# Performance work log

Hardware: AMD Instinct MI355X
Metric: run time of the kernel (lower is better)

Reference implementation:

```python
import jax, jax.numpy as jnp
import numpy as np

HIDDEN = 1024
HEADS = 16
HEAD_DIM = HIDDEN // HEADS


def setup_inputs() -> dict:
    key = jax.random.key(0)
    ks = jax.random.split(key, 9)
    B, S = 4, 2048
    s = 1.0 / np.sqrt(HIDDEN)
    return {
        "inputs": jax.random.normal(ks[0], (B, S, HIDDEN), dtype=jnp.float32),
        "Wq": jax.random.normal(ks[1], (HIDDEN, HIDDEN), dtype=jnp.float32) * s,
        "bq": jnp.zeros((HIDDEN,), dtype=jnp.float32),
        "Wk": jax.random.normal(ks[2], (HIDDEN, HIDDEN), dtype=jnp.float32) * s,
        "bk": jnp.zeros((HIDDEN,), dtype=jnp.float32),
        "Wv": jax.random.normal(ks[3], (HIDDEN, HIDDEN), dtype=jnp.float32) * s,
        "bv": jnp.zeros((HIDDEN,), dtype=jnp.float32),
        "Wp": jax.random.normal(ks[4], (HIDDEN, HIDDEN), dtype=jnp.float32) * s,
        "bp": jnp.zeros((HIDDEN,), dtype=jnp.float32),
        "heads_z": jnp.ones((1, HEADS, 1, 1), dtype=jnp.float32),
        "hidden_z": jnp.ones((HIDDEN,), dtype=jnp.float32),
    }


def _split_heads(x):
    # [B,S,HIDDEN] -> [B,H,S,Dh]
    B, S, _ = x.shape
    return x.reshape(B, S, HEADS, HEAD_DIM).transpose(0, 2, 1, 3)


def reference(inputs, Wq, bq, Wk, bk, Wv, bv, Wp, bp, heads_z, hidden_z):
    q = _split_heads(inputs @ Wq.T + bq)
    k = _split_heads(inputs @ Wk.T + bk)
    v = _split_heads(inputs @ Wv.T + bv)
    scores = jnp.einsum("bhqd,bhkd->bhqk", q, k) / jnp.sqrt(
        jnp.asarray(HEAD_DIM, dtype=q.dtype))
    probs = jax.nn.softmax(scores, axis=-1)
    ctx = jnp.einsum("bhqk,bhkd->bhqd", probs, v)  # [B,H,S,Dh]
    ctx = ctx * heads_z
    B, H, S, D = ctx.shape
    ctx = ctx.transpose(0, 2, 1, 3).reshape(B, S, H * D)
    out = ctx @ Wp.T + bp
    out = out * hidden_z
    return out
```

## Files before the change

kernel.cpp:

```cpp
#include <hip/hip_runtime.h>
#include <hip/hip_bf16.h>

#define HID 1024
#define NH 16
#define DH 64
#define SEQ 2048
#define NB 4
#define MTOT (NB*SEQ)

typedef __attribute__((ext_vector_type(4))) float f32x4;
typedef __attribute__((ext_vector_type(8))) __bf16 bf16x8;
typedef __attribute__((ext_vector_type(4))) __bf16 bf16x4;

__device__ __forceinline__ f32x4 mfma16(bf16x8 a, bf16x8 b, f32x4 c) {
    return __builtin_amdgcn_mfma_f32_16x16x32_bf16(a, b, c, 0, 0, 0);
}

__device__ __forceinline__ void gload16(const void* g, void* l) {
    __builtin_amdgcn_global_load_lds(
        (const __attribute__((address_space(1))) unsigned int*)g,
        (__attribute__((address_space(3))) unsigned int*)l, 16, 0, 0);
}

__device__ __forceinline__ float fexp2(float x) {
#if __has_builtin(__builtin_amdgcn_exp2f)
    return __builtin_amdgcn_exp2f(x);
#else
    return exp2f(x);
#endif
}

__global__ __launch_bounds__(256)
void cvt(const float* __restrict__ in, __bf16* __restrict__ out, int n) {
    int i = (blockIdx.x * 256 + threadIdx.x) * 4;
    if (i >= n) return;
    float4 v = *(const float4*)(in + i);
    bf16x4 o = { (__bf16)v.x, (__bf16)v.y, (__bf16)v.z, (__bf16)v.w };
    *(bf16x4*)(out + i) = o;
}

template<int MODE>
__global__ __launch_bounds__(256)
void gemm_bt(const __bf16* __restrict__ A, const __bf16* __restrict__ W,
             const float* __restrict__ bias, const float* __restrict__ hz,
             void* __restrict__ outp)
{
    __shared__ __bf16 As[128 * 32];
    __shared__ __bf16 Bs[128 * 32];
    const int tid  = threadIdx.x;
    const int lane = tid & 63, wid = tid >> 6;
    const int m0 = blockIdx.x * 128;
    const int n0 = blockIdx.y * 128;
    const int wm = (wid >> 1) * 64, wn = (wid & 1) * 64;

    f32x4 acc[4][4];
    #pragma unroll
    for (int i = 0; i < 4; i++)
        #pragma unroll
        for (int j = 0; j < 4; j++) acc[i][j] = (f32x4){0.f, 0.f, 0.f, 0.f};

    for (int kt = 0; kt < HID; kt += 32) {
        #pragma unroll
        for (int i = 0; i < 2; i++) {
            int c = wid * 128 + i * 64 + lane;
            int row = c >> 2, slot = c & 3;
            int ss = slot ^ (row & 3);
            gload16(A + (size_t)(m0 + row) * HID + kt + ss * 8, (char*)As + c * 16);
            gload16(W + (size_t)(n0 + row) * HID + kt + ss * 8, (char*)Bs + c * 16);
        }
        __syncthreads();

        bf16x8 af[4], bfr[4];
        #pragma unroll
        for (int mi = 0; mi < 4; mi++) {
            int row = wm + mi * 16 + (lane & 15);
            int off = row * 64 + (((lane >> 4) * 16) ^ ((row & 3) << 4));
            af[mi] = *(const bf16x8*)((const char*)As + off);
        }
        #pragma unroll
        for (int ni = 0; ni < 4; ni++) {
            int row = wn + ni * 16 + (lane & 15);
            int off = row * 64 + (((lane >> 4) * 16) ^ ((row & 3) << 4));
            bfr[ni] = *(const bf16x8*)((const char*)Bs + off);
        }
        #pragma unroll
        for (int mi = 0; mi < 4; mi++)
            #pragma unroll
            for (int ni = 0; ni < 4; ni++)
                acc[mi][ni] = mfma16(af[mi], bfr[ni], acc[mi][ni]);
        __syncthreads();
    }

    #pragma unroll
    for (int mi = 0; mi < 4; mi++)
        #pragma unroll
        for (int ni = 0; ni < 4; ni++)
            #pragma unroll
            for (int r = 0; r < 4; r++) {
                int m = m0 + wm + mi * 16 + ((lane >> 4) * 4) + r;
                int n = n0 + wn + ni * 16 + (lane & 15);
                float v = acc[mi][ni][r] + bias[n];
                if (MODE == 3) {
                    ((float*)outp)[(size_t)m * HID + n] = v * hz[n];
                } else {
                    int b = m >> 11, s = m & (SEQ - 1);
                    int h = n >> 6,  d = n & 63;
                    size_t idx;
                    if (MODE == 2) idx = ((size_t)(b * NH + h) * DH + d) * SEQ + s;
                    else           idx = ((size_t)(b * NH + h) * SEQ + s) * DH + d;
                    ((__bf16*)outp)[idx] = (__bf16)v;
                }
            }
}

#define KVB 64
#define SM_SCALE 0.18033688f

__global__ __launch_bounds__(512, 4)
void attn(const __bf16* __restrict__ Q, const __bf16* __restrict__ K,
          const __bf16* __restrict__ VT, const float* __restrict__ heads_z,
          __bf16* __restrict__ C)
{
    __shared__ __bf16 Ks[2][KVB * 64];
    __shared__ __bf16 Vs[2][KVB * 64];
    __shared__ __bf16 Ps[8][32 * 64];
    const int tid = threadIdx.x, lane = tid & 63, wid = tid >> 6;
    const int qb = blockIdx.x, h = blockIdx.y, b = blockIdx.z;
    const size_t bh = (size_t)(b * NH + h);
    const __bf16* Qg = Q + bh * SEQ * DH;
    const __bf16* Kg = K + bh * SEQ * DH;
    const __bf16* Vg = VT + bh * (size_t)DH * SEQ;
    const int q0 = qb * 256;

    bf16x8 qa[2][2];
    #pragma unroll
    for (int mi = 0; mi < 2; mi++)
        #pragma unroll
        for (int kf = 0; kf < 2; kf++) {
            int row = q0 + wid * 32 + mi * 16 + (lane & 15);
            qa[mi][kf] = *(const bf16x8*)(Qg + (size_t)row * DH + kf * 32 + (lane >> 4) * 8);
        }

    f32x4 ctx[2][4];
    float mrun[2] = {-1e30f, -1e30f}, lrun[2] = {0.f, 0.f};
    #pragma unroll
    for (int mi = 0; mi < 2; mi++)
        #pragma unroll
        for (int ni = 0; ni < 4; ni++) ctx[mi][ni] = (f32x4){0.f, 0.f, 0.f, 0.f};

    const int sc_row = tid >> 3, sc_slot = tid & 7;
    const int sc_ss = sc_slot ^ (sc_row & 7);

    gload16(Kg + (size_t)sc_row * DH + sc_ss * 8, (char*)&Ks[0][0] + tid * 16);
    gload16(Vg + (size_t)sc_row * SEQ + 0 + sc_ss * 8, (char*)&Vs[0][0] + tid * 16);
    __syncthreads();

    int cur = 0;
    for (int kv0 = 0; kv0 < SEQ; kv0 += KVB) {
        if (kv0 + KVB < SEQ) {
            gload16(Kg + (size_t)(kv0 + KVB + sc_row) * DH + sc_ss * 8,
                    (char*)&Ks[cur ^ 1][0] + tid * 16);
            gload16(Vg + (size_t)sc_row * SEQ + (kv0 + KVB) + sc_ss * 8,
                    (char*)&Vs[cur ^ 1][0] + tid * 16);
        }

        bf16x8 kb[4][2];
        #pragma unroll
        for (int ni = 0; ni < 4; ni++)
            #pragma unroll
            for (int kf = 0; kf < 2; kf++) {
                int row = ni * 16 + (lane & 15);
                int off = row * 128 + ((kf * 64 + (lane >> 4) * 16) ^ ((row & 7) << 4));
                kb[ni][kf] = *(const bf16x8*)((const char*)&Ks[cur][0] + off);
            }
        f32x4 st[2][4];
        #pragma unroll
        for (int mi = 0; mi < 2; mi++)
            #pragma unroll
            for (int ni = 0; ni < 4; ni++) {
                f32x4 t = (f32x4){0.f, 0.f, 0.f, 0.f};
                t = mfma16(kb[ni][0], qa[mi][0], t);
                t = mfma16(kb[ni][1], qa[mi][1], t);
                st[mi][ni] = t;
            }

        #pragma unroll
        for (int mi = 0; mi < 2; mi++) {
            float pm = st[mi][0][0];
            #pragma unroll
            for (int ni = 0; ni < 4; ni++)
                #pragma unroll
                for (int r = 0; r < 4; r++) pm = fmaxf(pm, st[mi][ni][r]);
            pm = fmaxf(pm, __shfl_xor(pm, 16));
            pm = fmaxf(pm, __shfl_xor(pm, 32));
            pm *= SM_SCALE;
            if (!__all(pm <= mrun[mi] + 8.f)) {
                float nm = fmaxf(mrun[mi], pm);
                float al = fexp2(mrun[mi] - nm);
                lrun[mi] *= al;
                mrun[mi] = nm;
                #pragma unroll
                for (int ni = 0; ni < 4; ni++) ctx[mi][ni] *= al;
            }
            float rs = 0.f;
            const float mneg = -mrun[mi];
            #pragma unroll
            for (int ni = 0; ni < 4; ni++) {
                bf16x4 pb;
                #pragma unroll
                for (int r = 0; r < 4; r++) {
                    float p = fexp2(fmaf(st[mi][ni][r], SM_SCALE, mneg));
                    rs += p;
                    pb[r] = (__bf16)p;
                }
                int row = mi * 16 + (lane & 15);
                int byte = row * 128 + ((32 * ni + 8 * (lane >> 4)) ^ ((row & 7) << 4));
                *(bf16x4*)((char*)&Ps[wid][0] + byte) = pb;
            }
            rs += __shfl_xor(rs, 16);
            rs += __shfl_xor(rs, 32);
            lrun[mi] += rs;
        }

        bf16x8 vb[4][2], pf[2][2];
        #pragma unroll
        for (int ni = 0; ni < 4; ni++)
            #pragma unroll
            for (int kf = 0; kf < 2; kf++) {
                int row = ni * 16 + (lane & 15);
                int off = row * 128 + ((kf * 64 + (lane >> 4) * 16) ^ ((row & 7) << 4));
                vb[ni][kf] = *(const bf16x8*)((const char*)&Vs[cur][0] + off);
            }
        #pragma unroll
        for (int mi = 0; mi < 2; mi++)
            #pragma unroll
            for (int kf = 0; kf < 2; kf++) {
                int row = mi * 16 + (lane & 15);
                int byte = row * 128 + ((16 * (lane >> 4) + 64 * kf) ^ ((row & 7) << 4));
                pf[mi][kf] = *(const bf16x8*)((const char*)&Ps[wid][0] + byte);
            }
        #pragma unroll
        for (int mi = 0; mi < 2; mi++)
            #pragma unroll
            for (int ni = 0; ni < 4; ni++) {
                ctx[mi][ni] = mfma16(vb[ni][0], pf[mi][0], ctx[mi][ni]);
                ctx[mi][ni] = mfma16(vb[ni][1], pf[mi][1], ctx[mi][ni]);
            }

        __syncthreads();
        cur ^= 1;
    }

    const float hzv = heads_z[h];
    #pragma unroll
    for (int mi = 0; mi < 2; mi++) {
        float rl = hzv / lrun[mi];
        int q = q0 + wid * 32 + mi * 16 + (lane & 15);
        #pragma unroll
        for (int ni = 0; ni < 4; ni++) {
            bf16x4 o;
            #pragma unroll
            for (int r = 0; r < 4; r++) o[r] = (__bf16)(ctx[mi][ni][r] * rl);
            int d = ni * 16 + (lane >> 4) * 4;
            *(bf16x4*)(C + (size_t)(b * SEQ + q) * HID + h * DH + d) = o;
        }
    }
}

extern "C" void kernel_launch(void* const* d_in, const int* in_sizes, int n_in,
                              void* d_out, int out_size, void* d_ws, size_t ws_size,
                              hipStream_t stream)
{
    const float* X    = (const float*)d_in[0];
    const float* Wq   = (const float*)d_in[1];
    const float* bq   = (const float*)d_in[2];
    const float* Wk   = (const float*)d_in[3];
    const float* bk   = (const float*)d_in[4];
    const float* Wv   = (const float*)d_in[5];
    const float* bv   = (const float*)d_in[6];
    const float* Wp   = (const float*)d_in[7];
    const float* bp   = (const float*)d_in[8];
    const float* hz   = (const float*)d_in[9];
    const float* hidz = (const float*)d_in[10];

    __bf16* ws  = (__bf16*)d_ws;
    __bf16* Xb  = ws;
    __bf16* Wqb = Xb  + (size_t)MTOT * HID;
    __bf16* Wkb = Wqb + (size_t)HID * HID;
    __bf16* Wvb = Wkb + (size_t)HID * HID;
    __bf16* Wpb = Wvb + (size_t)HID * HID;
    __bf16* Qb  = Wpb + (size_t)HID * HID;
    __bf16* Kb  = Qb  + (size_t)MTOT * HID;
    __bf16* VTb = Kb  + (size_t)MTOT * HID;
    __bf16* Cb  = VTb + (size_t)MTOT * HID;

    cvt<<<(MTOT * HID / 4 + 255) / 256, 256, 0, stream>>>(X,  Xb,  MTOT * HID);
    cvt<<<(HID * HID / 4 + 255) / 256, 256, 0, stream>>>(Wq, Wqb, HID * HID);
    cvt<<<(HID * HID / 4 + 255) / 256, 256, 0, stream>>>(Wk, Wkb, HID * HID);
    cvt<<<(HID * HID / 4 + 255) / 256, 256, 0, stream>>>(Wv, Wvb, HID * HID);
    cvt<<<(HID * HID / 4 + 255) / 256, 256, 0, stream>>>(Wp, Wpb, HID * HID);

    dim3 gg(MTOT / 128, HID / 128);
    gemm_bt<0><<<gg, 256, 0, stream>>>(Xb, Wqb, bq, nullptr, Qb);
    gemm_bt<1><<<gg, 256, 0, stream>>>(Xb, Wkb, bk, nullptr, Kb);
    gemm_bt<2><<<gg, 256, 0, stream>>>(Xb, Wvb, bv, nullptr, VTb);

    attn<<<dim3(SEQ / 256, NH, NB), 512, 0, stream>>>(Qb, Kb, VTb, hz, Cb);

    gemm_bt<3><<<gg, 256, 0, stream>>>(Cb, Wpb, bp, hidz, d_out);
}
```

Measured before the change: 220.9 us.

## Use 32x32 MFMA in attention and keep P in registers via permlane swap

```diff
diff --git a/kernel.cpp b/kernel.cpp
--- a/kernel.cpp
+++ b/kernel.cpp
@@ -9,11 +9,17 @@
 #define MTOT (NB*SEQ)
 
 typedef __attribute__((ext_vector_type(4))) float f32x4;
+typedef __attribute__((ext_vector_type(16))) float f32x16;
 typedef __attribute__((ext_vector_type(8))) __bf16 bf16x8;
 typedef __attribute__((ext_vector_type(4))) __bf16 bf16x4;
+typedef __attribute__((ext_vector_type(2))) __bf16 bf16x2;
+typedef __attribute__((ext_vector_type(2))) int i32x2;
 
 __device__ __forceinline__ f32x4 mfma16(bf16x8 a, bf16x8 b, f32x4 c) {
     return __builtin_amdgcn_mfma_f32_16x16x32_bf16(a, b, c, 0, 0, 0);
+}
+__device__ __forceinline__ f32x16 mfma32(bf16x8 a, bf16x8 b, f32x16 c) {
+    return __builtin_amdgcn_mfma_f32_32x32x16_bf16(a, b, c, 0, 0, 0);
 }
 
 __device__ __forceinline__ void gload16(const void* g, void* l) {
@@ -28,6 +34,36 @@
 #else
     return exp2f(x);
 #endif
+}
+
+__device__ __forceinline__ unsigned pkbf2(float lo, float hi) {
+    union { bf16x2 v; unsigned u; } c;
+    c.v = (bf16x2){ (__bf16)lo, (__bf16)hi };
+    return c.u;
+}
+
+__device__ __forceinline__ void swap32(unsigned &a, unsigned &b) {
+#if __has_builtin(__builtin_amdgcn_permlane32_swap)
+    i32x2 r = __builtin_amdgcn_permlane32_swap((int)a, (int)b, false, false);
+    a = (unsigned)r.x; b = (unsigned)r.y;
+#else
+    const bool hi = (threadIdx.x & 32) != 0;
+    unsigned ta = __shfl_xor(a, 32), tb = __shfl_xor(b, 32);
+    unsigned na = hi ? tb : a;
+    unsigned nb = hi ? b : ta;
+    a = na; b = nb;
+#endif
+}
+
+__device__ __forceinline__ float swapmaxf(float x) {
+    unsigned a = __float_as_uint(x), b = a;
+    swap32(a, b);
+    return fmaxf(__uint_as_float(a), __uint_as_float(b));
+}
+__device__ __forceinline__ float swapaddf(float x) {
+    unsigned a = __float_as_uint(x), b = a;
+    swap32(a, b);
+    return __uint_as_float(a) + __uint_as_float(b);
 }
 
 __global__ __launch_bounds__(256)
@@ -123,30 +159,25 @@
 {
     __shared__ __bf16 Ks[2][KVB * 64];
     __shared__ __bf16 Vs[2][KVB * 64];
-    __shared__ __bf16 Ps[8][32 * 64];
     const int tid = threadIdx.x, lane = tid & 63, wid = tid >> 6;
-    const int qb = blockIdx.x, h = blockIdx.y, b = blockIdx.z;
-    const size_t bh = (size_t)(b * NH + h);
+    const int lh = lane >> 5;
+    const int qb = blockIdx.x, hd = blockIdx.y, b = blockIdx.z;
+    const size_t bh = (size_t)(b * NH + hd);
     const __bf16* Qg = Q + bh * SEQ * DH;
     const __bf16* Kg = K + bh * SEQ * DH;
     const __bf16* Vg = VT + bh * (size_t)DH * SEQ;
     const int q0 = qb * 256;
-
-    bf16x8 qa[2][2];
-    #pragma unroll
-    for (int mi = 0; mi < 2; mi++)
-        #pragma unroll
-        for (int kf = 0; kf < 2; kf++) {
-            int row = q0 + wid * 32 + mi * 16 + (lane & 15);
-            qa[mi][kf] = *(const bf16x8*)(Qg + (size_t)row * DH + kf * 32 + (lane >> 4) * 8);
-        }
-
-    f32x4 ctx[2][4];
-    float mrun[2] = {-1e30f, -1e30f}, lrun[2] = {0.f, 0.f};
-    #pragma unroll
-    for (int mi = 0; mi < 2; mi++)
-        #pragma unroll
-        for (int ni = 0; ni < 4; ni++) ctx[mi][ni] = (f32x4){0.f, 0.f, 0.f, 0.f};
+    const int q = q0 + wid * 32 + (lane & 31);
+
+    bf16x8 qf[4];
+    #pragma unroll
+    for (int s = 0; s < 4; s++)
+        qf[s] = *(const bf16x8*)(Qg + (size_t)q * DH + s * 16 + lh * 8);
+
+    f32x16 ctx0, ctx1;
+    #pragma unroll
+    for (int r = 0; r < 16; r++) { ctx0[r] = 0.f; ctx1[r] = 0.f; }
+    float mrun = -1e30f, lrun = 0.f;
 
     const int sc_row = tid >> 3, sc_slot = tid & 7;
     const int sc_ss = sc_slot ^ (sc_row & 7);
@@ -164,106 +195,97 @@
                     (char*)&Vs[cur ^ 1][0] + tid * 16);
         }
 
-        bf16x8 kb[4][2];
-        #pragma unroll
-        for (int ni = 0; ni < 4; ni++)
+        f32x16 st0, st1;
+        #pragma unroll
+        for (int r = 0; r < 16; r++) { st0[r] = 0.f; st1[r] = 0.f; }
+        const char* Kb = (const char*)&Ks[cur][0];
+        __builtin_amdgcn_s_setprio(1);
+        #pragma unroll
+        for (int s = 0; s < 4; s++) {
+            int r0 = lane & 31, r1 = r0 + 32;
+            int slot = 2 * s + lh;
+            bf16x8 k0 = *(const bf16x8*)(Kb + r0 * 128 + ((slot ^ (r0 & 7)) << 4));
+            bf16x8 k1 = *(const bf16x8*)(Kb + r1 * 128 + ((slot ^ (r1 & 7)) << 4));
+            st0 = mfma32(k0, qf[s], st0);
+            st1 = mfma32(k1, qf[s], st1);
+        }
+        __builtin_amdgcn_s_setprio(0);
+
+        float pm = st0[0];
+        #pragma unroll
+        for (int r = 1; r < 16; r++) pm = fmaxf(pm, st0[r]);
+        #pragma unroll
+        for (int r = 0; r < 16; r++) pm = fmaxf(pm, st1[r]);
+        pm = swapmaxf(pm);
+        pm *= SM_SCALE;
+        if (!__all(pm <= mrun + 8.f)) {
+            float nm = fmaxf(mrun, pm);
+            float al = fexp2(mrun - nm);
+            lrun *= al; mrun = nm;
             #pragma unroll
-            for (int kf = 0; kf < 2; kf++) {
-                int row = ni * 16 + (lane & 15);
-                int off = row * 128 + ((kf * 64 + (lane >> 4) * 16) ^ ((row & 7) << 4));
-                kb[ni][kf] = *(const bf16x8*)((const char*)&Ks[cur][0] + off);
-            }
-        f32x4 st[2][4];
-        #pragma unroll
-        for (int mi = 0; mi < 2; mi++)
-            #pragma unroll
-            for (int ni = 0; ni < 4; ni++) {
-                f32x4 t = (f32x4){0.f, 0.f, 0.f, 0.f};
-                t = mfma16(kb[ni][0], qa[mi][0], t);
-                t = mfma16(kb[ni][1], qa[mi][1], t);
-                st[mi][ni] = t;
-            }
-
-        #pragma unroll
-        for (int mi = 0; mi < 2; mi++) {
-            float pm = st[mi][0][0];
-            #pragma unroll
-            for (int ni = 0; ni < 4; ni++)
-                #pragma unroll
-                for (int r = 0; r < 4; r++) pm = fmaxf(pm, st[mi][ni][r]);
-            pm = fmaxf(pm, __shfl_xor(pm, 16));
-            pm = fmaxf(pm, __shfl_xor(pm, 32));
-            pm *= SM_SCALE;
-            if (!__all(pm <= mrun[mi] + 8.f)) {
-                float nm = fmaxf(mrun[mi], pm);
-                float al = fexp2(mrun[mi] - nm);
-                lrun[mi] *= al;
-                mrun[mi] = nm;
-                #pragma unroll
-                for (int ni = 0; ni < 4; ni++) ctx[mi][ni] *= al;
-            }
-            float rs = 0.f;
-            const float mneg = -mrun[mi];
-            #pragma unroll
-            for (int ni = 0; ni < 4; ni++) {
-                bf16x4 pb;
-                #pragma unroll
-                for (int r = 0; r < 4; r++) {
-                    float p = fexp2(fmaf(st[mi][ni][r], SM_SCALE, mneg));
-                    rs += p;
-                    pb[r] = (__bf16)p;
-                }
-                int row = mi * 16 + (lane & 15);
-                int byte = row * 128 + ((32 * ni + 8 * (lane >> 4)) ^ ((row & 7) << 4));
-                *(bf16x4*)((char*)&Ps[wid][0] + byte) = pb;
-            }
-            rs += __shfl_xor(rs, 16);
-            rs += __shfl_xor(rs, 32);
-            lrun[mi] += rs;
-        }
-
-        bf16x8 vb[4][2], pf[2][2];
-        #pragma unroll
-        for (int ni = 0; ni < 4; ni++)
-            #pragma unroll
-            for (int kf = 0; kf < 2; kf++) {
-                int row = ni * 16 + (lane & 15);
-                int off = row * 128 + ((kf * 64 + (lane >> 4) * 16) ^ ((row & 7) << 4));
-                vb[ni][kf] = *(const bf16x8*)((const char*)&Vs[cur][0] + off);
-            }
-        #pragma unroll
-        for (int mi = 0; mi < 2; mi++)
-            #pragma unroll
-            for (int kf = 0; kf < 2; kf++) {
-                int row = mi * 16 + (lane & 15);
-                int byte = row * 128 + ((16 * (lane >> 4) + 64 * kf) ^ ((row & 7) << 4));
-                pf[mi][kf] = *(const bf16x8*)((const char*)&Ps[wid][0] + byte);
-            }
-        #pragma unroll
-        for (int mi = 0; mi < 2; mi++)
-            #pragma unroll
-            for (int ni = 0; ni < 4; ni++) {
-                ctx[mi][ni] = mfma16(vb[ni][0], pf[mi][0], ctx[mi][ni]);
-                ctx[mi][ni] = mfma16(vb[ni][1], pf[mi][1], ctx[mi][ni]);
-            }
+            for (int r = 0; r < 16; r++) { ctx0[r] *= al; ctx1[r] *= al; }
+        }
+        float rs = 0.f;
+        const float mneg = -mrun;
+        #pragma unroll
+        for (int r = 0; r < 16; r++) {
+            float e0 = fexp2(fmaf(st0[r], SM_SCALE, mneg));
+            float e1 = fexp2(fmaf(st1[r], SM_SCALE, mneg));
+            st0[r] = e0; st1[r] = e1;
+            rs += e0 + e1;
+        }
+        lrun += swapaddf(rs);
+
+        unsigned X0 = pkbf2(st0[0],  st0[1]),  X1 = pkbf2(st0[2],  st0[3]);
+        unsigned X2 = pkbf2(st0[4],  st0[5]),  X3 = pkbf2(st0[6],  st0[7]);
+        unsigned X4 = pkbf2(st0[8],  st0[9]),  X5 = pkbf2(st0[10], st0[11]);
+        unsigned X6 = pkbf2(st0[12], st0[13]), X7 = pkbf2(st0[14], st0[15]);
+        unsigned Y0 = pkbf2(st1[0],  st1[1]),  Y1 = pkbf2(st1[2],  st1[3]);
+        unsigned Y2 = pkbf2(st1[4],  st1[5]),  Y3 = pkbf2(st1[6],  st1[7]);
+        unsigned Y4 = pkbf2(st1[8],  st1[9]),  Y5 = pkbf2(st1[10], st1[11]);
+        unsigned Y6 = pkbf2(st1[12], st1[13]), Y7 = pkbf2(st1[14], st1[15]);
+        swap32(X0, X2); swap32(X1, X3);
+        swap32(X4, X6); swap32(X5, X7);
+        swap32(Y0, Y2); swap32(Y1, Y3);
+        swap32(Y4, Y6); swap32(Y5, Y7);
+        union W4 { unsigned w[4]; bf16x8 v; };
+        W4 pf[4];
+        pf[0].w[0]=X0; pf[0].w[1]=X1; pf[0].w[2]=X2; pf[0].w[3]=X3;
+        pf[1].w[0]=X4; pf[1].w[1]=X5; pf[1].w[2]=X6; pf[1].w[3]=X7;
+        pf[2].w[0]=Y0; pf[2].w[1]=Y1; pf[2].w[2]=Y2; pf[2].w[3]=Y3;
+        pf[3].w[0]=Y4; pf[3].w[1]=Y5; pf[3].w[2]=Y6; pf[3].w[3]=Y7;
+
+        const char* Vb = (const char*)&Vs[cur][0];
+        __builtin_amdgcn_s_setprio(1);
+        #pragma unroll
+        for (int s = 0; s < 4; s++) {
+            int r0 = lane & 31, r1 = r0 + 32;
+            int slot = 2 * s + lh;
+            bf16x8 v0 = *(const bf16x8*)(Vb + r0 * 128 + ((slot ^ (r0 & 7)) << 4));
+            bf16x8 v1 = *(const bf16x8*)(Vb + r1 * 128 + ((slot ^ (r1 & 7)) << 4));
+            ctx0 = mfma32(v0, pf[s].v, ctx0);
+            ctx1 = mfma32(v1, pf[s].v, ctx1);
+        }
+        __builtin_amdgcn_s_setprio(0);
 
         __syncthreads();
         cur ^= 1;
     }
 
-    const float hzv = heads_z[h];
-    #pragma unroll
-    for (int mi = 0; mi < 2; mi++) {
-        float rl = hzv / lrun[mi];
-        int q = q0 + wid * 32 + mi * 16 + (lane & 15);
-        #pragma unroll
-        for (int ni = 0; ni < 4; ni++) {
-            bf16x4 o;
-            #pragma unroll
-            for (int r = 0; r < 4; r++) o[r] = (__bf16)(ctx[mi][ni][r] * rl);
-            int d = ni * 16 + (lane >> 4) * 4;
-            *(bf16x4*)(C + (size_t)(b * SEQ + q) * HID + h * DH + d) = o;
-        }
+    const float hzv = heads_z[hd];
+    const float rl = hzv / lrun;
+    __bf16* Crow = C + (size_t)(b * SEQ + q) * HID + hd * DH;
+    #pragma unroll
+    for (int g = 0; g < 4; g++) {
+        bf16x4 o0, o1;
+        #pragma unroll
+        for (int j = 0; j < 4; j++) {
+            o0[j] = (__bf16)(ctx0[4 * g + j] * rl);
+            o1[j] = (__bf16)(ctx1[4 * g + j] * rl);
+        }
+        int d0 = 8 * g + 4 * lh;
+        *(bf16x4*)(Crow + d0) = o0;
+        *(bf16x4*)(Crow + 32 + d0) = o1;
     }
 }
 
```

Result: no change. 220.3 us (-0.3%).
